# Kernel optimization log

Hardware: AMD Instinct MI355X
Metric: run time of the kernel (lower is better)

## Reference

```python
import jax, jax.numpy as jnp
import numpy as np

N = 100000      # nodes
E = 3200000     # edges
F = 128         # input features
H = 16          # hiddenSize (hard-coded in source)
C = 10          # num_classes
RATIO = 0.25
K1 = int(np.ceil(RATIO * N))   # 25000 nodes kept by pool1
K2 = int(np.ceil(RATIO * K1))  # 6250 nodes kept by pool2


def gcn_conv(x, W, b, src, dst, ew, n):
    """PyG GCNConv: add self-loops (weight 1), symmetric normalization.
    ew carries edge validity mask / weights; ew=0 edges are exactly equivalent
    to removed edges (contribute nothing to degree or aggregation)."""
    h = x @ W                                                   # [n, out]
    deg = jax.ops.segment_sum(ew, dst, num_segments=n) + 1.0    # +1 self-loop
    dinv = jax.lax.rsqrt(deg)
    norm = dinv[src] * dinv[dst] * ew                           # [E]
    agg = jax.ops.segment_sum(h[src] * norm[:, None], dst, num_segments=n)
    agg = agg + h * (dinv * dinv)[:, None]                      # self-loop msg
    return agg + b


def graph_conv_score(x, wroot, wrel, b, src, dst, ew, n):
    """PyG GraphConv (SAGPooling default GNN) with out_channels=1:
    score_i = x_i @ Wroot + (sum_j x_j) @ Wrel + b."""
    agg = jax.ops.segment_sum(x[src] * ew[:, None], dst, num_segments=n)
    return (x @ wroot + agg @ wrel + b).reshape(-1)             # [n]


def sag_pool(x, src, dst, ew, wroot, wrel, b, n, k):
    """SAGPooling: score -> top-k -> x[perm]*tanh(score[perm]) -> filter_adj.
    filter_adj is expressed by relabeling kept nodes and zeroing dropped edges
    (math-identical to edge removal for downstream GCN/GraphConv)."""
    score = graph_conv_score(x, wroot, wrel, b, src, dst, ew, n)
    vals, perm = jax.lax.top_k(score, k)
    xp = x[perm] * jnp.tanh(vals)[:, None]
    new_idx = jnp.full((n,), -1, dtype=jnp.int32).at[perm].set(
        jnp.arange(k, dtype=jnp.int32))
    ns, nd = new_idx[src], new_idx[dst]
    valid = (ns >= 0) & (nd >= 0)
    new_ew = jnp.where(valid, ew, 0.0)
    ns = jnp.where(valid, ns, 0)
    nd = jnp.where(valid, nd, 0)
    return xp, ns, nd, new_ew


def setup_inputs() -> dict:
    key = jax.random.key(0)
    ks = jax.random.split(key, 9)
    s = 0.1
    return {
        "x": jax.random.normal(ks[0], (N, F), jnp.float32),
        "edge_src": jax.random.randint(ks[1], (E,), 0, N, dtype=jnp.int32),
        "edge_dst": jax.random.randint(ks[2], (E,), 0, N, dtype=jnp.int32),
        "W1": jax.random.normal(ks[3], (F, H), jnp.float32) * s,
        "b1": jnp.zeros((H,), jnp.float32),
        "p1_wroot": jax.random.normal(ks[4], (H, 1), jnp.float32) * s,
        "p1_wrel": jax.random.normal(ks[5], (H, 1), jnp.float32) * s,
        "p1_b": jnp.zeros((1,), jnp.float32),
        "W2": jax.random.normal(ks[6], (H, C), jnp.float32) * s,
        "b2": jnp.zeros((C,), jnp.float32),
        "p2_wroot": jax.random.normal(ks[7], (C, 1), jnp.float32) * s,
        "p2_wrel": jax.random.normal(ks[8], (C, 1), jnp.float32) * s,
        "p2_b": jnp.zeros((1,), jnp.float32),
    }


def reference(x, edge_src, edge_dst, W1, b1, p1_wroot, p1_wrel, p1_b,
              W2, b2, p2_wroot, p2_wrel, p2_b):
    ew0 = jnp.ones((E,), x.dtype)
    # conv1 + relu (dropout is identity in eval mode)
    h = jax.nn.relu(gcn_conv(x, W1, b1, edge_src, edge_dst, ew0, N))
    # pool1 (ratio 0.25)
    x1, s1, d1, ew1 = sag_pool(h, edge_src, edge_dst, ew0,
                               p1_wroot, p1_wrel, p1_b, N, K1)
    # conv2
    h2 = gcn_conv(x1, W2, b2, s1, d1, ew1, K1)
    # pool2 (ratio 0.25)
    x2, s2, d2, ew2 = sag_pool(h2, s1, d1, ew1,
                               p2_wroot, p2_wrel, p2_b, K1, K2)
    # global mean pool over the single graph, then log_softmax
    out = jnp.mean(x2, axis=0, keepdims=True)   # [1, C]
    return jax.nn.log_softmax(out, axis=1)
```

## Files before the change

### kernel.cpp

```cpp
#include <hip/hip_runtime.h>
#include <math.h>

#define NN 100000
#define EE 3200000
#define FF 128
#define HH 16
#define CC 10
#define PC 12
#define KK1 25000
#define KK2 6250

#define NBIN 512
#define BUCK_SHIFT 8
#define BUCK_MASK 255
#define ABLK 256
#define EPB (EE / ABLK)
#define NBUCK ((NN + 255) / 256)

struct SelState {
  unsigned prefix;
  unsigned kcur;
  unsigned ctr_gt;
  unsigned ctr_eq;
  unsigned hist[256];
};

__device__ __forceinline__ unsigned fkey(float f) {
  unsigned u = __float_as_uint(f);
  return (u & 0x80000000u) ? ~u : (u | 0x80000000u);
}

__global__ __launch_bounds__(256) void k_xw1(const float* __restrict__ x,
                                             const float* __restrict__ W1,
                                             float* __restrict__ h0) {
  __shared__ float sW[FF * HH];
  __shared__ float sx[16][FF];
  int t = threadIdx.x;
  for (int i = t; i < FF * HH; i += 256) sW[i] = W1[i];
  int base = blockIdx.x * 16;
  for (int i = t; i < 16 * FF; i += 256) {
    int r = i >> 7, c = i & 127;
    int node = base + r;
    sx[r][c] = (node < NN) ? x[(size_t)node * FF + c] : 0.f;
  }
  __syncthreads();
  int r = t >> 4;
  int o = t & 15;
  float acc = 0.f;
#pragma unroll
  for (int k = 0; k < FF; ++k) acc += sx[r][k] * sW[k * HH + o];
  int node = base + r;
  if (node < NN) h0[node * HH + o] = acc;
}

__global__ __launch_bounds__(256) void k_bhist(const int* __restrict__ dst,
                                               unsigned* __restrict__ Hist) {
  __shared__ unsigned sh[NBIN];
  int t = threadIdx.x;
  for (int i = t; i < NBIN; i += 256) sh[i] = 0;
  __syncthreads();
  int base = blockIdx.x * EPB;
  for (int i = base + t; i < base + EPB; i += 256)
    atomicAdd(&sh[dst[i] >> BUCK_SHIFT], 1u);
  __syncthreads();
  for (int i = t; i < NBIN; i += 256) Hist[blockIdx.x * NBIN + i] = sh[i];
}

__global__ __launch_bounds__(64) void k_bcursor(unsigned* __restrict__ Hist,
                                                unsigned* __restrict__ Tot) {
  int bin = blockIdx.x * 64 + threadIdx.x;
  unsigned run = 0;
#pragma unroll 8
  for (int b = 0; b < ABLK; ++b) {
    unsigned c = Hist[b * NBIN + bin];
    Hist[b * NBIN + bin] = run;
    run += c;
  }
  Tot[bin] = run;
}

__global__ __launch_bounds__(512) void k_bscan(const unsigned* __restrict__ Tot,
                                               unsigned* __restrict__ BucketOff) {
  __shared__ unsigned s[NBIN];
  int t = threadIdx.x;
  unsigned v = Tot[t];
  s[t] = v;
  __syncthreads();
  for (int off = 1; off < NBIN; off <<= 1) {
    unsigned u = (t >= off) ? s[t - off] : 0;
    __syncthreads();
    s[t] += u;
    __syncthreads();
  }
  BucketOff[t] = s[t] - v;
  if (t == NBIN - 1) BucketOff[NBIN] = s[t];
}

__global__ __launch_bounds__(256) void k_bscatter(const int* __restrict__ src,
                                                  const int* __restrict__ dst,
                                                  const unsigned* __restrict__ Hist,
                                                  const unsigned* __restrict__ BucketOff,
                                                  unsigned* __restrict__ packed) {
  __shared__ unsigned cur[NBIN];
  int t = threadIdx.x;
  for (int i = t; i < NBIN; i += 256)
    cur[i] = BucketOff[i] + Hist[blockIdx.x * NBIN + i];
  __syncthreads();
  int base = blockIdx.x * EPB;
  for (int i = base + t; i < base + EPB; i += 256) {
    int d = dst[i];
    unsigned pos = atomicAdd(&cur[d >> BUCK_SHIFT], 1u);
    packed[pos] = ((unsigned)(d & BUCK_MASK) << 17) | (unsigned)src[i];
  }
}

__global__ __launch_bounds__(256) void k_bfine(const unsigned* __restrict__ packed,
                                               const unsigned* __restrict__ BucketOff,
                                               int* __restrict__ rowstart,
                                               float* __restrict__ dinv,
                                               int* __restrict__ csr) {
  __shared__ unsigned fcnt[256], fpos[256], fcur[256];
  int bin = blockIdx.x;
  int t = threadIdx.x;
  unsigned b0 = BucketOff[bin], b1 = BucketOff[bin + 1];
  fcnt[t] = 0;
  __syncthreads();
  for (unsigned e = b0 + t; e < b1; e += 256)
    atomicAdd(&fcnt[packed[e] >> 17], 1u);
  __syncthreads();
  unsigned v = fcnt[t];
  fpos[t] = v;
  __syncthreads();
  for (int off = 1; off < 256; off <<= 1) {
    unsigned u = (t >= off) ? fpos[t - off] : 0;
    __syncthreads();
    fpos[t] += u;
    __syncthreads();
  }
  unsigned excl = fpos[t] - v;
  fcur[t] = b0 + excl;
  int node = bin * 256 + t;
  if (node < NN) {
    rowstart[node] = (int)(b0 + excl);
    dinv[node] = rsqrtf((float)v + 1.0f);
  }
  if (bin == 0 && t == 0) rowstart[NN] = EE;
  __syncthreads();
  for (unsigned e = b0 + t; e < b1; e += 256) {
    unsigned p = packed[e];
    unsigned pos = atomicAdd(&fcur[p >> 17], 1u);
    csr[pos] = (int)(p & 0x1FFFFu);
  }
}

__global__ __launch_bounds__(256) void k_conv1(const float* __restrict__ h0,
                                               const float* __restrict__ dinv,
                                               const int* __restrict__ rowstart,
                                               const int* __restrict__ csr,
                                               const float* __restrict__ b1,
                                               const float* __restrict__ wroot,
                                               const float* __restrict__ wrel,
                                               const float* __restrict__ bp,
                                               float* __restrict__ h,
                                               float* __restrict__ score,
                                               float* __restrict__ hrel) {
  int node = blockIdx.x * 4 + (threadIdx.x >> 6);
  if (node >= NN) return;
  int lane = threadIdx.x & 63;
  int eslot = lane >> 2;
  int kq = lane & 3;
  int s0 = rowstart[node], s1 = rowstart[node + 1];
  float ax = 0.f, ay = 0.f, az = 0.f, aw = 0.f;
  for (int base = s0; base < s1; base += 16) {
    int idx = base + eslot;
    bool on = idx < s1;
    int sv = on ? csr[idx] : 0;
    float dv = on ? dinv[sv] : 0.f;
    float4 hv = *(const float4*)(h0 + sv * HH + kq * 4);
    ax += hv.x * dv;
    ay += hv.y * dv;
    az += hv.z * dv;
    aw += hv.w * dv;
  }
#pragma unroll
  for (int m = 4; m <= 32; m <<= 1) {
    ax += __shfl_xor(ax, m);
    ay += __shfl_xor(ay, m);
    az += __shfl_xor(az, m);
    aw += __shfl_xor(aw, m);
  }
  float di = dinv[node];
  float4 hs = *(const float4*)(h0 + node * HH + kq * 4);
  float vx = ax * di + hs.x * di * di + b1[kq * 4 + 0];
  float vy = ay * di + hs.y * di * di + b1[kq * 4 + 1];
  float vz = az * di + hs.z * di * di + b1[kq * 4 + 2];
  float vw = aw * di + hs.w * di * di + b1[kq * 4 + 3];
  vx = vx > 0.f ? vx : 0.f;
  vy = vy > 0.f ? vy : 0.f;
  vz = vz > 0.f ? vz : 0.f;
  vw = vw > 0.f ? vw : 0.f;
  if (eslot == 0) {
    float4 o4 = make_float4(vx, vy, vz, vw);
    *(float4*)(h + node * HH + kq * 4) = o4;
  }
  float sr = vx * wroot[kq * 4] + vy * wroot[kq * 4 + 1] +
             vz * wroot[kq * 4 + 2] + vw * wroot[kq * 4 + 3];
  float sl = vx * wrel[kq * 4] + vy * wrel[kq * 4 + 1] +
             vz * wrel[kq * 4 + 2] + vw * wrel[kq * 4 + 3];
  sr += __shfl_xor(sr, 1);
  sr += __shfl_xor(sr, 2);
  sl += __shfl_xor(sl, 1);
  sl += __shfl_xor(sl, 2);
  if (lane == 0) {
    score[node] = sr + bp[0];
    hrel[node] = sl;
  }
}

__global__ __launch_bounds__(256) void k_scoreg(const int* __restrict__ rowstart,
                                                const int* __restrict__ csr,
                                                const float* __restrict__ hrel,
                                                float* __restrict__ score) {
  int node = blockIdx.x * 16 + (threadIdx.x >> 4);
  if (node >= NN) return;
  int lane = threadIdx.x & 15;
  int s0 = rowstart[node], s1 = rowstart[node + 1];
  float sum = 0.f;
  for (int e = s0 + lane; e < s1; e += 16) sum += hrel[csr[e]];
#pragma unroll
  for (int m = 8; m; m >>= 1) sum += __shfl_xor(sum, m, 16);
  if (lane == 0) score[node] += sum;
}

__global__ void k_state_init(SelState* st, int K) {
  if (threadIdx.x == 0) {
    st->prefix = 0;
    st->kcur = (unsigned)K;
    st->ctr_gt = 0;
    st->ctr_eq = 0;
  }
  st->hist[threadIdx.x] = 0;
}

__global__ __launch_bounds__(256) void k_hist(const float* __restrict__ vals, int n,
                                              SelState* st, int pass) {
  __shared__ unsigned sh[256];
  int t = threadIdx.x;
  sh[t] = 0;
  __syncthreads();
  int i = blockIdx.x * 256 + t;
  if (i < n) {
    unsigned key = fkey(vals[i]);
    bool ok = true;
    if (pass != 0) ok = (key >> (32 - 8 * pass)) == st->prefix;
    if (ok) atomicAdd(&sh[(key >> (24 - 8 * pass)) & 255], 1u);
  }
  __syncthreads();
  if (sh[t]) atomicAdd(&st->hist[t], sh[t]);
}

__global__ __launch_bounds__(256) void k_scan(SelState* st) {
  __shared__ unsigned s[256];
  int t = threadIdx.x;
  unsigned kcur = st->kcur;
  unsigned v = st->hist[t];
  s[t] = v;
  __syncthreads();
  for (int off = 1; off < 256; off <<= 1) {
    unsigned u = (t + off < 256) ? s[t + off] : 0;
    __syncthreads();
    s[t] += u;
    __syncthreads();
  }
  unsigned Sme = s[t];
  unsigned Snext = (t < 255) ? s[t + 1] : 0;
  if (Sme >= kcur && Snext < kcur) {
    st->prefix = (st->prefix << 8) | (unsigned)t;
    st->kcur = kcur - Snext;
  }
  st->hist[t] = 0;
}

__global__ void k_select1(const float* __restrict__ score, const float* __restrict__ h,
                          SelState* st, int* __restrict__ new_idx,
                          int* __restrict__ orig_of, float* __restrict__ x1) {
  int i = blockIdx.x * blockDim.x + threadIdx.x;
  if (i >= NN) return;
  float sc = score[i];
  unsigned key = fkey(sc);
  unsigned T = st->prefix;
  int id = -1;
  if (key > T) {
    id = (int)atomicAdd(&st->ctr_gt, 1u);
  } else if (key == T) {
    unsigned p = atomicAdd(&st->ctr_eq, 1u);
    unsigned kneed = st->kcur;
    if (p < kneed) id = (KK1 - (int)kneed) + (int)p;
  }
  new_idx[i] = id;
  if (id >= 0) {
    orig_of[id] = i;
    float tv = tanhf(sc);
#pragma unroll
    for (int k = 0; k < HH; ++k) x1[id * HH + k] = h[i * HH + k] * tv;
  }
}

__global__ __launch_bounds__(256) void k_deg2(const int* __restrict__ orig_of,
                                              const int* __restrict__ rowstart,
                                              const int* __restrict__ csr,
                                              const int* __restrict__ nidx,
                                              float* __restrict__ dinv2) {
  int j = blockIdx.x * 16 + (threadIdx.x >> 4);
  if (j >= KK1) return;
  int lane = threadIdx.x & 15;
  int o = orig_of[j];
  int s0 = rowstart[o], s1 = rowstart[o + 1];
  int c = 0;
  for (int e = s0 + lane; e < s1; e += 16) c += (nidx[csr[e]] >= 0) ? 1 : 0;
#pragma unroll
  for (int m = 8; m; m >>= 1) c += __shfl_xor(c, m, 16);
  if (lane == 0) dinv2[j] = rsqrtf((float)c + 1.0f);
}

__global__ void k_xw2(const float* __restrict__ x1, const float* __restrict__ W2,
                      float* __restrict__ h20) {
  int t = blockIdx.x * blockDim.x + threadIdx.x;
  if (t >= KK1 * PC) return;
  int node = t / PC;
  int o = t - node * PC;
  float acc = 0.f;
  if (o < CC) {
#pragma unroll
    for (int k = 0; k < HH; ++k) acc += x1[node * HH + k] * W2[k * CC + o];
  }
  h20[t] = acc;
}

__global__ __launch_bounds__(256) void k_conv2(const float* __restrict__ h20,
                                               const float* __restrict__ dinv2,
                                               const int* __restrict__ orig_of,
                                               const int* __restrict__ rowstart,
                                               const int* __restrict__ csr,
                                               const int* __restrict__ nidx,
                                               const float* __restrict__ b2,
                                               const float* __restrict__ wroot,
                                               const float* __restrict__ wrel,
                                               const float* __restrict__ bp,
                                               float* __restrict__ h2,
                                               float* __restrict__ score2,
                                               float* __restrict__ h2rel) {
  int j = blockIdx.x * 4 + (threadIdx.x >> 6);
  if (j >= KK1) return;
  int lane = threadIdx.x & 63;
  int eslot = lane >> 2;
  int kq = lane & 3;
  int o = orig_of[j];
  int s0 = rowstart[o], s1 = rowstart[o + 1];
  float ax = 0.f, ay = 0.f, az = 0.f, aw = 0.f;
  for (int base = s0; base < s1; base += 16) {
    int idx = base + eslot;
    bool on = idx < s1;
    int sv = on ? nidx[csr[idx]] : -1;
    float dv = (sv >= 0) ? dinv2[sv] : 0.f;
    int sva = (sv >= 0) ? sv : 0;
    float4 hv = *(const float4*)(h20 + sva * PC + ((kq < 3) ? kq * 4 : 8));
    if (kq == 3) dv = 0.f;
    ax += hv.x * dv;
    ay += hv.y * dv;
    az += hv.z * dv;
    aw += hv.w * dv;
  }
#pragma unroll
  for (int m = 4; m <= 32; m <<= 1) {
    ax += __shfl_xor(ax, m);
    ay += __shfl_xor(ay, m);
    az += __shfl_xor(az, m);
    aw += __shfl_xor(aw, m);
  }
  float di = dinv2[j];
  int kb = (kq < 3) ? kq * 4 : 8;
  float4 hs = *(const float4*)(h20 + j * PC + kb);
  float bx = (kb + 0 < CC) ? b2[kb + 0] : 0.f;
  float by = (kb + 1 < CC) ? b2[kb + 1] : 0.f;
  float bz = (kb + 2 < CC) ? b2[kb + 2] : 0.f;
  float bw = (kb + 3 < CC) ? b2[kb + 3] : 0.f;
  float vx = ax * di + hs.x * di * di + bx;
  float vy = ay * di + hs.y * di * di + by;
  float vz = az * di + hs.z * di * di + bz;
  float vw = aw * di + hs.w * di * di + bw;
  if (kq == 3) { vx = vy = vz = vw = 0.f; }
  if (kb + 2 >= CC) vz = 0.f;
  if (kb + 3 >= CC) vw = 0.f;
  if (eslot == 0 && kq < 3) {
    float4 o4 = make_float4(vx, vy, vz, vw);
    *(float4*)(h2 + j * PC + kq * 4) = o4;
  }
  float wrx = (kb + 0 < CC) ? wroot[kb + 0] : 0.f;
  float wry = (kb + 1 < CC) ? wroot[kb + 1] : 0.f;
  float wrz = (kb + 2 < CC) ? wroot[kb + 2] : 0.f;
  float wrw = (kb + 3 < CC) ? wroot[kb + 3] : 0.f;
  float wlx = (kb + 0 < CC) ? wrel[kb + 0] : 0.f;
  float wly = (kb + 1 < CC) ? wrel[kb + 1] : 0.f;
  float wlz = (kb + 2 < CC) ? wrel[kb + 2] : 0.f;
  float wlw = (kb + 3 < CC) ? wrel[kb + 3] : 0.f;
  float sr = (kq == 3) ? 0.f : (vx * wrx + vy * wry + vz * wrz + vw * wrw);
  float sl = (kq == 3) ? 0.f : (vx * wlx + vy * wly + vz * wlz + vw * wlw);
  sr += __shfl_xor(sr, 1);
  sr += __shfl_xor(sr, 2);
  sl += __shfl_xor(sl, 1);
  sl += __shfl_xor(sl, 2);
  if (lane == 0) {
    score2[j] = sr + bp[0];
    h2rel[j] = sl;
  }
}

__global__ __launch_bounds__(256) void k_score2g(const int* __restrict__ orig_of,
                                                 const int* __restrict__ rowstart,
                                                 const int* __restrict__ csr,
                                                 const int* __restrict__ nidx,
                                                 const float* __restrict__ h2rel,
                                                 float* __restrict__ score2) {
  int j = blockIdx.x * 16 + (threadIdx.x >> 4);
  if (j >= KK1) return;
  int lane = threadIdx.x & 15;
  int o = orig_of[j];
  int s0 = rowstart[o], s1 = rowstart[o + 1];
  float sum = 0.f;
  for (int e = s0 + lane; e < s1; e += 16) {
    int s = nidx[csr[e]];
    if (s >= 0) sum += h2rel[s];
  }
#pragma unroll
  for (int m = 8; m; m >>= 1) sum += __shfl_xor(sum, m, 16);
  if (lane == 0) score2[j] += sum;
}

__global__ __launch_bounds__(256) void k_final_accum(const float* __restrict__ score,
                                                     const float* __restrict__ h2,
                                                     SelState* st, float* __restrict__ acc) {
  int i = blockIdx.x * blockDim.x + threadIdx.x;
  float tv = 0.f;
  if (i < KK1) {
    float sc = score[i];
    unsigned key = fkey(sc);
    unsigned T = st->prefix;
    bool keep = false;
    if (key > T) {
      keep = true;
    } else if (key == T) {
      unsigned p = atomicAdd(&st->ctr_eq, 1u);
      keep = (p < st->kcur);
    }
    if (keep) tv = tanhf(sc);
  }
  __shared__ float sacc[CC];
  if (threadIdx.x < CC) sacc[threadIdx.x] = 0.f;
  __syncthreads();
#pragma unroll
  for (int c = 0; c < CC; ++c) {
    float v = (i < KK1 && tv != 0.f) ? h2[i * PC + c] * tv : 0.f;
#pragma unroll
    for (int m = 32; m; m >>= 1) v += __shfl_xor(v, m, 64);
    if ((threadIdx.x & 63) == 0) atomicAdd(&sacc[c], v);
  }
  __syncthreads();
  if (threadIdx.x < CC) atomicAdd(&acc[threadIdx.x], sacc[threadIdx.x]);
}

__global__ void k_final(const float* __restrict__ acc, float* __restrict__ out) {
  if (threadIdx.x != 0 || blockIdx.x != 0) return;
  float v[CC];
  float m = -1e30f;
#pragma unroll
  for (int c = 0; c < CC; ++c) {
    v[c] = acc[c] / (float)KK2;
    if (v[c] > m) m = v[c];
  }
  float s = 0.f;
#pragma unroll
  for (int c = 0; c < CC; ++c) s += expf(v[c] - m);
  float l = logf(s);
#pragma unroll
  for (int c = 0; c < CC; ++c) out[c] = v[c] - m - l;
}

extern "C" void kernel_launch(void* const* d_in, const int* in_sizes, int n_in,
                              void* d_out, int out_size, void* d_ws, size_t ws_size,
                              hipStream_t stream) {
  const float* x      = (const float*)d_in[0];
  const int*   esrc   = (const int*)d_in[1];
  const int*   edst   = (const int*)d_in[2];
  const float* W1     = (const float*)d_in[3];
  const float* b1     = (const float*)d_in[4];
  const float* w1root = (const float*)d_in[5];
  const float* w1rel  = (const float*)d_in[6];
  const float* p1b    = (const float*)d_in[7];
  const float* W2     = (const float*)d_in[8];
  const float* b2     = (const float*)d_in[9];
  const float* w2root = (const float*)d_in[10];
  const float* w2rel  = (const float*)d_in[11];
  const float* p2b    = (const float*)d_in[12];
  float* out = (float*)d_out;

  char* w = (char*)d_ws;
  size_t off = 0;
  auto alloc = [&](size_t bytes) -> char* {
    char* p = w + off;
    off += (bytes + 255) & ~(size_t)255;
    return p;
  };
  float*    h0      = (float*)alloc((size_t)NN * HH * 4);
  float*    hbuf    = (float*)alloc((size_t)NN * HH * 4);
  float*    dinv1   = (float*)alloc((size_t)NN * 4);
  float*    hrel1   = (float*)alloc((size_t)NN * 4);
  float*    score1  = (float*)alloc((size_t)NN * 4);
  int*      nidx    = (int*)  alloc((size_t)NN * 4);
  int*      csr     = (int*)  alloc((size_t)EE * 4);
  unsigned* packed  = (unsigned*)alloc((size_t)EE * 4);
  int*      rowst   = (int*)  alloc((size_t)(NN + 1) * 4);
  unsigned* Hist    = (unsigned*)alloc((size_t)ABLK * NBIN * 4);
  unsigned* Tot     = (unsigned*)alloc((size_t)NBIN * 4);
  unsigned* BOff    = (unsigned*)alloc((size_t)(NBIN + 1) * 4);
  SelState* st1     = (SelState*)alloc(sizeof(SelState));
  SelState* st2     = (SelState*)alloc(sizeof(SelState));
  float*    acc     = (float*)alloc(256);

  size_t off2 = 0;
  auto alloc2 = [&](size_t bytes) -> char* {
    char* p = (char*)h0 + off2;
    off2 += (bytes + 255) & ~(size_t)255;
    return p;
  };
  float* x1      = (float*)alloc2((size_t)KK1 * HH * 4);
  float* h20     = (float*)alloc2((size_t)KK1 * PC * 4 + 256);
  float* h2      = (float*)alloc2((size_t)KK1 * PC * 4 + 256);
  float* dinv2   = (float*)alloc2((size_t)KK1 * 4);
  float* h2rel   = (float*)alloc2((size_t)KK1 * 4);
  float* score2  = (float*)alloc2((size_t)KK1 * 4);
  int*   orig_of = (int*)  alloc2((size_t)KK1 * 4);

  const int BN  = (NN + 255) / 256;
  const int BK1 = (KK1 + 255) / 256;

  k_xw1<<<NN / 16, 256, 0, stream>>>(x, W1, h0);

  k_bhist<<<ABLK, 256, 0, stream>>>(edst, Hist);
  k_bcursor<<<NBIN / 64, 64, 0, stream>>>(Hist, Tot);
  k_bscan<<<1, NBIN, 0, stream>>>(Tot, BOff);
  k_bscatter<<<ABLK, 256, 0, stream>>>(esrc, edst, Hist, BOff, packed);
  k_bfine<<<NBUCK, 256, 0, stream>>>(packed, BOff, rowst, dinv1, csr);

  k_conv1<<<(NN + 3) / 4, 256, 0, stream>>>(h0, dinv1, rowst, csr, b1, w1root, w1rel,
                                            p1b, hbuf, score1, hrel1);
  k_scoreg<<<(NN + 15) / 16, 256, 0, stream>>>(rowst, csr, hrel1, score1);

  k_state_init<<<1, 256, 0, stream>>>(st1, KK1);
  for (int p = 0; p < 4; ++p) {
    k_hist<<<BN, 256, 0, stream>>>(score1, NN, st1, p);
    k_scan<<<1, 256, 0, stream>>>(st1);
  }
  k_select1<<<BN, 256, 0, stream>>>(score1, hbuf, st1, nidx, orig_of, x1);

  k_deg2<<<(KK1 + 15) / 16, 256, 0, stream>>>(orig_of, rowst, csr, nidx, dinv2);
  k_xw2<<<(KK1 * PC + 255) / 256, 256, 0, stream>>>(x1, W2, h20);
  k_conv2<<<(KK1 + 3) / 4, 256, 0, stream>>>(h20, dinv2, orig_of, rowst, csr, nidx,
                                             b2, w2root, w2rel, p2b, h2, score2, h2rel);
  k_score2g<<<(KK1 + 15) / 16, 256, 0, stream>>>(orig_of, rowst, csr, nidx, h2rel, score2);

  k_state_init<<<1, 256, 0, stream>>>(st2, KK2);
  for (int p = 0; p < 4; ++p) {
    k_hist<<<BK1, 256, 0, stream>>>(score2, KK1, st2, p);
    k_scan<<<1, 256, 0, stream>>>(st2);
  }
  hipMemsetAsync(acc, 0, CC * 4, stream);
  k_final_accum<<<BK1, 256, 0, stream>>>(score2, h2, st2, acc);
  k_final<<<1, 64, 0, stream>>>(acc, out);
}
```

Before: 477.9 us.

## Fuse radix top-k histogram and scan via last-block pattern, merge deg2/xw2

Replaces the 4-pass 8-bit radix select (separate histogram and single-block scan kernels, plus a state-init kernel) with 3 passes of 11/11/10-bit bins. The last block to finish each pass does the scan, found through an atomic done-counter, so the scan launches and state-init disappear. It also merges the deg2 and xw2 kernels into one launch and splits the conv1 gather loop into two independent accumulators for more memory-level parallelism. This cuts roughly a dozen small serialized launches, at the cost of larger shared histograms and a global done-counter/threadfence protocol, which relies on the up-front memset for correctness.

```diff
diff --git a/kernel.cpp b/kernel.cpp
--- a/kernel.cpp
+++ b/kernel.cpp
@@ -17,12 +17,15 @@
 #define EPB (EE / ABLK)
 #define NBUCK ((NN + 255) / 256)
 
-struct SelState {
+#define DEG2_BLKS ((KK1 + 15) / 16)
+#define XW2_BLKS ((KK1 * PC + 255) / 256)
+
+struct TopkCtl {
   unsigned prefix;
   unsigned kcur;
   unsigned ctr_gt;
   unsigned ctr_eq;
-  unsigned hist[256];
+  unsigned done0, done1, done2, pad;
 };
 
 __device__ __forceinline__ unsigned fkey(float f) {
@@ -171,17 +174,21 @@
   int kq = lane & 3;
   int s0 = rowstart[node], s1 = rowstart[node + 1];
   float ax = 0.f, ay = 0.f, az = 0.f, aw = 0.f;
-  for (int base = s0; base < s1; base += 16) {
-    int idx = base + eslot;
-    bool on = idx < s1;
-    int sv = on ? csr[idx] : 0;
-    float dv = on ? dinv[sv] : 0.f;
-    float4 hv = *(const float4*)(h0 + sv * HH + kq * 4);
-    ax += hv.x * dv;
-    ay += hv.y * dv;
-    az += hv.z * dv;
-    aw += hv.w * dv;
-  }
+  float bx_ = 0.f, by_ = 0.f, bz_ = 0.f, bw_ = 0.f;
+  for (int base = s0; base < s1; base += 32) {
+    int i1 = base + eslot;
+    int i2 = base + 16 + eslot;
+    bool on1 = i1 < s1, on2 = i2 < s1;
+    int sv1 = on1 ? csr[i1] : 0;
+    int sv2 = on2 ? csr[i2] : 0;
+    float dv1 = on1 ? dinv[sv1] : 0.f;
+    float dv2 = on2 ? dinv[sv2] : 0.f;
+    float4 h1 = *(const float4*)(h0 + sv1 * HH + kq * 4);
+    float4 h2v = *(const float4*)(h0 + sv2 * HH + kq * 4);
+    ax += h1.x * dv1; ay += h1.y * dv1; az += h1.z * dv1; aw += h1.w * dv1;
+    bx_ += h2v.x * dv2; by_ += h2v.y * dv2; bz_ += h2v.z * dv2; bw_ += h2v.w * dv2;
+  }
+  ax += bx_; ay += by_; az += bz_; aw += bw_;
 #pragma unroll
   for (int m = 4; m <= 32; m <<= 1) {
     ax += __shfl_xor(ax, m);
@@ -232,57 +239,82 @@
   if (lane == 0) score[node] += sum;
 }
 
-__global__ void k_state_init(SelState* st, int K) {
-  if (threadIdx.x == 0) {
-    st->prefix = 0;
-    st->kcur = (unsigned)K;
-    st->ctr_gt = 0;
-    st->ctr_eq = 0;
-  }
-  st->hist[threadIdx.x] = 0;
-}
-
-__global__ __launch_bounds__(256) void k_hist(const float* __restrict__ vals, int n,
-                                              SelState* st, int pass) {
-  __shared__ unsigned sh[256];
+template <int PASS>
+__global__ __launch_bounds__(256) void k_topk_pass(const float* __restrict__ vals,
+                                                   int n, int K, TopkCtl* ctl,
+                                                   unsigned* __restrict__ ghist,
+                                                   int nblocks) {
+  const int NB = (PASS == 2) ? 1024 : 2048;
+  __shared__ unsigned sh[2048];
   int t = threadIdx.x;
-  sh[t] = 0;
-  __syncthreads();
-  int i = blockIdx.x * 256 + t;
-  if (i < n) {
+  for (int i = t; i < NB; i += 256) sh[i] = 0;
+  unsigned prefix = 0, kcur = (unsigned)K;
+  if (PASS > 0) {
+    prefix = __hip_atomic_load(&ctl->prefix, __ATOMIC_RELAXED, __HIP_MEMORY_SCOPE_AGENT);
+    kcur = __hip_atomic_load(&ctl->kcur, __ATOMIC_RELAXED, __HIP_MEMORY_SCOPE_AGENT);
+  }
+  __syncthreads();
+  for (int i = blockIdx.x * 256 + t; i < n; i += nblocks * 256) {
     unsigned key = fkey(vals[i]);
-    bool ok = true;
-    if (pass != 0) ok = (key >> (32 - 8 * pass)) == st->prefix;
-    if (ok) atomicAdd(&sh[(key >> (24 - 8 * pass)) & 255], 1u);
-  }
-  __syncthreads();
-  if (sh[t]) atomicAdd(&st->hist[t], sh[t]);
-}
-
-__global__ __launch_bounds__(256) void k_scan(SelState* st) {
-  __shared__ unsigned s[256];
-  int t = threadIdx.x;
-  unsigned kcur = st->kcur;
-  unsigned v = st->hist[t];
-  s[t] = v;
+    bool ok;
+    unsigned bin;
+    if (PASS == 0) { ok = true; bin = key >> 21; }
+    else if (PASS == 1) { ok = (key >> 21) == prefix; bin = (key >> 10) & 2047u; }
+    else { ok = (key >> 10) == prefix; bin = key & 1023u; }
+    if (ok) atomicAdd(&sh[bin], 1u);
+  }
+  __syncthreads();
+  for (int i = t; i < NB; i += 256) if (sh[i]) atomicAdd(&ghist[i], sh[i]);
+  __threadfence();
+  __shared__ unsigned lastflag;
+  if (t == 0) {
+    unsigned* done = (PASS == 0) ? &ctl->done0 : (PASS == 1) ? &ctl->done1 : &ctl->done2;
+    unsigned old = atomicAdd(done, 1u);
+    lastflag = (old == (unsigned)(nblocks - 1)) ? 1u : 0u;
+  }
+  __syncthreads();
+  if (!lastflag) return;
+  __threadfence();
+  const int PER = NB / 256;
+  unsigned loc[8];
+  unsigned psum = 0;
+#pragma unroll
+  for (int j = 0; j < PER; ++j) {
+    loc[j] = __hip_atomic_load(&ghist[t * PER + j], __ATOMIC_RELAXED,
+                               __HIP_MEMORY_SCOPE_AGENT);
+    psum += loc[j];
+  }
+  __shared__ unsigned ss[256];
+  ss[t] = psum;
   __syncthreads();
   for (int off = 1; off < 256; off <<= 1) {
-    unsigned u = (t + off < 256) ? s[t + off] : 0;
+    unsigned u = (t + off < 256) ? ss[t + off] : 0;
     __syncthreads();
-    s[t] += u;
+    ss[t] += u;
     __syncthreads();
   }
-  unsigned Sme = s[t];
-  unsigned Snext = (t < 255) ? s[t + 1] : 0;
-  if (Sme >= kcur && Snext < kcur) {
-    st->prefix = (st->prefix << 8) | (unsigned)t;
-    st->kcur = kcur - Snext;
-  }
-  st->hist[t] = 0;
+  unsigned above = (t < 255) ? ss[t + 1] : 0;
+  unsigned run = above;
+  int winner = -1;
+  unsigned newk = 0;
+  for (int j = PER - 1; j >= 0; --j) {
+    unsigned tot = run + loc[j];
+    if (tot >= kcur && run < kcur) { winner = t * PER + j; newk = kcur - run; }
+    run = tot;
+  }
+  if (winner >= 0) {
+    unsigned npfx = (PASS == 0) ? (unsigned)winner
+                  : (PASS == 1) ? ((prefix << 11) | (unsigned)winner)
+                                : ((prefix << 10) | (unsigned)winner);
+    __hip_atomic_store(&ctl->prefix, npfx, __ATOMIC_RELAXED, __HIP_MEMORY_SCOPE_AGENT);
+    __hip_atomic_store(&ctl->kcur, newk, __ATOMIC_RELAXED, __HIP_MEMORY_SCOPE_AGENT);
+  }
+  for (int i = t; i < 2048; i += 256)
+    __hip_atomic_store(&ghist[i], 0u, __ATOMIC_RELAXED, __HIP_MEMORY_SCOPE_AGENT);
 }
 
 __global__ void k_select1(const float* __restrict__ score, const float* __restrict__ h,
-                          SelState* st, int* __restrict__ new_idx,
+                          TopkCtl* st, int* __restrict__ new_idx,
                           int* __restrict__ orig_of, float* __restrict__ x1) {
   int i = blockIdx.x * blockDim.x + threadIdx.x;
   if (i >= NN) return;
@@ -306,35 +338,38 @@
   }
 }
 
-__global__ __launch_bounds__(256) void k_deg2(const int* __restrict__ orig_of,
-                                              const int* __restrict__ rowstart,
-                                              const int* __restrict__ csr,
-                                              const int* __restrict__ nidx,
-                                              float* __restrict__ dinv2) {
-  int j = blockIdx.x * 16 + (threadIdx.x >> 4);
-  if (j >= KK1) return;
-  int lane = threadIdx.x & 15;
-  int o = orig_of[j];
-  int s0 = rowstart[o], s1 = rowstart[o + 1];
-  int c = 0;
-  for (int e = s0 + lane; e < s1; e += 16) c += (nidx[csr[e]] >= 0) ? 1 : 0;
-#pragma unroll
-  for (int m = 8; m; m >>= 1) c += __shfl_xor(c, m, 16);
-  if (lane == 0) dinv2[j] = rsqrtf((float)c + 1.0f);
-}
-
-__global__ void k_xw2(const float* __restrict__ x1, const float* __restrict__ W2,
-                      float* __restrict__ h20) {
-  int t = blockIdx.x * blockDim.x + threadIdx.x;
-  if (t >= KK1 * PC) return;
-  int node = t / PC;
-  int o = t - node * PC;
-  float acc = 0.f;
-  if (o < CC) {
-#pragma unroll
-    for (int k = 0; k < HH; ++k) acc += x1[node * HH + k] * W2[k * CC + o];
-  }
-  h20[t] = acc;
+__global__ __launch_bounds__(256) void k_deg2xw2(const int* __restrict__ orig_of,
+                                                 const int* __restrict__ rowstart,
+                                                 const int* __restrict__ csr,
+                                                 const int* __restrict__ nidx,
+                                                 float* __restrict__ dinv2,
+                                                 const float* __restrict__ x1,
+                                                 const float* __restrict__ W2,
+                                                 float* __restrict__ h20) {
+  int b = blockIdx.x;
+  if (b < DEG2_BLKS) {
+    int j = b * 16 + (threadIdx.x >> 4);
+    if (j >= KK1) return;
+    int lane = threadIdx.x & 15;
+    int o = orig_of[j];
+    int s0 = rowstart[o], s1 = rowstart[o + 1];
+    int c = 0;
+    for (int e = s0 + lane; e < s1; e += 16) c += (nidx[csr[e]] >= 0) ? 1 : 0;
+#pragma unroll
+    for (int m = 8; m; m >>= 1) c += __shfl_xor(c, m, 16);
+    if (lane == 0) dinv2[j] = rsqrtf((float)c + 1.0f);
+  } else {
+    int t = (b - DEG2_BLKS) * 256 + threadIdx.x;
+    if (t >= KK1 * PC) return;
+    int node = t / PC;
+    int o = t - node * PC;
+    float acc = 0.f;
+    if (o < CC) {
+#pragma unroll
+      for (int k = 0; k < HH; ++k) acc += x1[node * HH + k] * W2[k * CC + o];
+    }
+    h20[t] = acc;
+  }
 }
 
 __global__ __launch_bounds__(256) void k_conv2(const float* __restrict__ h20,
@@ -439,7 +474,7 @@
 
 __global__ __launch_bounds__(256) void k_final_accum(const float* __restrict__ score,
                                                      const float* __restrict__ h2,
-                                                     SelState* st, float* __restrict__ acc) {
+                                                     TopkCtl* st, float* __restrict__ acc) {
   int i = blockIdx.x * blockDim.x + threadIdx.x;
   float tv = 0.f;
   if (i < KK1) {
@@ -523,9 +558,11 @@
   unsigned* Hist    = (unsigned*)alloc((size_t)ABLK * NBIN * 4);
   unsigned* Tot     = (unsigned*)alloc((size_t)NBIN * 4);
   unsigned* BOff    = (unsigned*)alloc((size_t)(NBIN + 1) * 4);
-  SelState* st1     = (SelState*)alloc(sizeof(SelState));
-  SelState* st2     = (SelState*)alloc(sizeof(SelState));
-  float*    acc     = (float*)alloc(256);
+  char*     ctlreg  = alloc(8192 + 256);
+  unsigned* ghist   = (unsigned*)ctlreg;
+  TopkCtl*  ctl1    = (TopkCtl*)(ctlreg + 8192);
+  TopkCtl*  ctl2    = (TopkCtl*)(ctlreg + 8192 + 32);
+  float*    acc     = (float*)(ctlreg + 8192 + 64);
 
   size_t off2 = 0;
   auto alloc2 = [&](size_t bytes) -> char* {
@@ -544,6 +581,8 @@
   const int BN  = (NN + 255) / 256;
   const int BK1 = (KK1 + 255) / 256;
 
+  hipMemsetAsync(ctlreg, 0, 8192 + 256, stream);
+
   k_xw1<<<NN / 16, 256, 0, stream>>>(x, W1, h0);
 
   k_bhist<<<ABLK, 256, 0, stream>>>(edst, Hist);
@@ -556,25 +595,20 @@
                                             p1b, hbuf, score1, hrel1);
   k_scoreg<<<(NN + 15) / 16, 256, 0, stream>>>(rowst, csr, hrel1, score1);
 
-  k_state_init<<<1, 256, 0, stream>>>(st1, KK1);
-  for (int p = 0; p < 4; ++p) {
-    k_hist<<<BN, 256, 0, stream>>>(score1, NN, st1, p);
-    k_scan<<<1, 256, 0, stream>>>(st1);
-  }
-  k_select1<<<BN, 256, 0, stream>>>(score1, hbuf, st1, nidx, orig_of, x1);
-
-  k_deg2<<<(KK1 + 15) / 16, 256, 0, stream>>>(orig_of, rowst, csr, nidx, dinv2);
-  k_xw2<<<(KK1 * PC + 255) / 256, 256, 0, stream>>>(x1, W2, h20);
+  k_topk_pass<0><<<BN, 256, 0, stream>>>(score1, NN, KK1, ctl1, ghist, BN);
+  k_topk_pass<1><<<BN, 256, 0, stream>>>(score1, NN, KK1, ctl1, ghist, BN);
+  k_topk_pass<2><<<BN, 256, 0, stream>>>(score1, NN, KK1, ctl1, ghist, BN);
+  k_select1<<<BN, 256, 0, stream>>>(score1, hbuf, ctl1, nidx, orig_of, x1);
+
+  k_deg2xw2<<<DEG2_BLKS + XW2_BLKS, 256, 0, stream>>>(orig_of, rowst, csr, nidx,
+                                                      dinv2, x1, W2, h20);
   k_conv2<<<(KK1 + 3) / 4, 256, 0, stream>>>(h20, dinv2, orig_of, rowst, csr, nidx,
                                              b2, w2root, w2rel, p2b, h2, score2, h2rel);
   k_score2g<<<(KK1 + 15) / 16, 256, 0, stream>>>(orig_of, rowst, csr, nidx, h2rel, score2);
 
-  k_state_init<<<1, 256, 0, stream>>>(st2, KK2);
-  for (int p = 0; p < 4; ++p) {
-    k_hist<<<BK1, 256, 0, stream>>>(score2, KK1, st2, p);
-    k_scan<<<1, 256, 0, stream>>>(st2);
-  }
-  hipMemsetAsync(acc, 0, CC * 4, stream);
-  k_final_accum<<<BK1, 256, 0, stream>>>(score2, h2, st2, acc);
+  k_topk_pass<0><<<BK1, 256, 0, stream>>>(score2, KK1, KK2, ctl2, ghist, BK1);
+  k_topk_pass<1><<<BK1, 256, 0, stream>>>(score2, KK1, KK2, ctl2, ghist, BK1);
+  k_topk_pass<2><<<BK1, 256, 0, stream>>>(score2, KK1, KK2, ctl2, ghist, BK1);
+  k_final_accum<<<BK1, 256, 0, stream>>>(score2, h2, ctl2, acc);
   k_final<<<1, 64, 0, stream>>>(acc, out);
 }
```

Result: slower. 525.0 us (+9.9%).
